# Optimization experiments

Measured on AMD Instinct MI355X. Metric: run time of the kernel, lower is better.

Reference implementation:

```python
import jax, jax.numpy as jnp
import numpy as np

N_NODES = 100000
N_EDGES = 1600000
HEADS = 4
HID = 64
IN_CH = 3
N_GRAPHS = 64
NEG_SLOPE = 0.2  # PyG GATConv default


def _gat_layer(x, src, dst, W, a_src, a_dst, b):
    """PyG GATConv with concat=False (head-mean), eval mode (no dropout)."""
    N = x.shape[0]
    xl = (x @ W).reshape(N, HEADS, HID)            # [N,H,C]
    es = (xl * a_src).sum(-1)                       # [N,H] alpha_src
    ed = (xl * a_dst).sum(-1)                       # [N,H] alpha_dst
    e = jax.nn.leaky_relu(es[src] + ed[dst], NEG_SLOPE)  # [E,H]
    # segment softmax over incoming edges of each dst node
    m = jax.ops.segment_max(e, dst, num_segments=N)      # [N,H]
    ex = jnp.exp(e - m[dst])
    s = jax.ops.segment_sum(ex, dst, num_segments=N)     # [N,H]
    alpha = ex / s[dst]                                   # [E,H]
    msg = xl[src] * alpha[:, :, None]                     # [E,H,C]
    out = jax.ops.segment_sum(msg, dst, num_segments=N)   # [N,H,C]
    return out.mean(axis=1) + b                            # head mean + bias


def setup_inputs() -> dict:
    key = jax.random.key(0)
    ks = jax.random.split(key, 12)
    x = jax.random.normal(ks[0], (N_NODES, IN_CH), dtype=jnp.float32)
    edge_index = jax.random.randint(ks[1], (2, N_EDGES), 0, N_NODES, dtype=jnp.int64)
    batch_ids = jnp.sort(jax.random.randint(ks[2], (N_NODES,), 0, N_GRAPHS, dtype=jnp.int64))
    def glorot(k, shape, fan_in):
        return jax.random.normal(k, shape, dtype=jnp.float32) / np.sqrt(fan_in)
    W1 = glorot(ks[3], (IN_CH, HEADS * HID), IN_CH)
    a_src1 = glorot(ks[4], (HEADS, HID), HID)
    a_dst1 = glorot(ks[5], (HEADS, HID), HID)
    b1 = jnp.zeros((HID,), dtype=jnp.float32)
    W2 = glorot(ks[6], (HID, HEADS * HID), HID)
    a_src2 = glorot(ks[7], (HEADS, HID), HID)
    a_dst2 = glorot(ks[8], (HEADS, HID), HID)
    b2 = jnp.zeros((HID,), dtype=jnp.float32)
    return {"x": x, "edge_index": edge_index, "batch_ids": batch_ids,
            "W1": W1, "a_src1": a_src1, "a_dst1": a_dst1, "b1": b1,
            "W2": W2, "a_src2": a_src2, "a_dst2": a_dst2, "b2": b2}


def reference(x, edge_index, batch_ids, W1, a_src1, a_dst1, b1, W2, a_src2, a_dst2, b2):
    src, dst = edge_index[0], edge_index[1]
    h = jax.nn.relu(_gat_layer(x, src, dst, W1, a_src1, a_dst1, b1))
    h = jax.nn.relu(_gat_layer(h, src, dst, W2, a_src2, a_dst2, b2))
    # global_add_pool
    g = jax.ops.segment_sum(h, batch_ids, num_segments=N_GRAPHS)  # [G, HID]
    return g
```

## Files before the change

kernel.cpp:

```cpp
#include <hip/hip_runtime.h>
#include <math.h>

#define HEADS 4
#define HID 64
#define BSHIFT 7
#define BWIDTH 128
#define CCAP 4096
#define DCHUNK 8192

typedef __attribute__((ext_vector_type(8))) short short8;
typedef __attribute__((ext_vector_type(4))) float f32x4;
typedef __attribute__((ext_vector_type(2))) float f32x2;

__device__ __forceinline__ float lrelu(float x) { return x > 0.f ? x : 0.2f * x; }

__device__ __forceinline__ unsigned short bf16r(float f) {
    unsigned u = __float_as_uint(f);
    unsigned r = (u + 0x7FFFu + ((u >> 16) & 1u)) >> 16;
    return (unsigned short)r;
}
__device__ __forceinline__ f32x2 unpk(unsigned u) {
    f32x2 r;
    r.x = __uint_as_float(u << 16);
    r.y = __uint_as_float(u & 0xffff0000u);
    return r;
}

__device__ __forceinline__ float wred_sum(float v) {
#pragma unroll
    for (int o = 32; o > 0; o >>= 1) v += __shfl_xor(v, o);
    return v;
}
__device__ __forceinline__ float red16_sum(float v) {
#pragma unroll
    for (int o = 8; o > 0; o >>= 1) v += __shfl_xor(v, o);
    return v;
}

__global__ void k_bhist(const int* __restrict__ dstI, int* __restrict__ bcnt,
                        int E, int NBUCK) {
    __shared__ int h[1024];
    for (int i = threadIdx.x; i < NBUCK; i += 256) h[i] = 0;
    __syncthreads();
    int stride = gridDim.x * 256;
    for (int e = blockIdx.x * 256 + threadIdx.x; e < E; e += stride)
        atomicAdd(&h[dstI[e] >> BSHIFT], 1);
    __syncthreads();
    for (int i = threadIdx.x; i < NBUCK; i += 256)
        if (h[i]) atomicAdd(&bcnt[i], h[i]);
}

__global__ void k_bscan(const int* __restrict__ bcnt, int* __restrict__ bbase,
                        int* __restrict__ gcur, int* __restrict__ off,
                        int NBUCK, int N, int E) {
    __shared__ int lds[1024];
    int t = threadIdx.x;
    int v = (t < NBUCK) ? bcnt[t] : 0;
    lds[t] = v;
    __syncthreads();
    for (int s = 1; s < 1024; s <<= 1) {
        int u = (t >= s) ? lds[t - s] : 0;
        __syncthreads();
        lds[t] += u;
        __syncthreads();
    }
    if (t < NBUCK) {
        int b = lds[t] - v;
        bbase[t] = b;
        gcur[t] = b;
    }
    if (t == 0) { bbase[NBUCK] = E; off[N] = E; }
}

__global__ void k_bdist(const int* __restrict__ srcI, const int* __restrict__ dstI,
                        int* __restrict__ gcur, unsigned* __restrict__ pairs,
                        int E, int NBUCK) {
    __shared__ int h[1024];
    __shared__ int cur[1024];
    for (int i = threadIdx.x; i < NBUCK; i += 1024) h[i] = 0;
    __syncthreads();
    int base = blockIdx.x * DCHUNK;
    int sr[8], dr[8];
#pragma unroll
    for (int k = 0; k < 8; k++) {
        int e = base + threadIdx.x + k * 1024;
        if (e < E) {
            sr[k] = srcI[e];
            dr[k] = dstI[e];
            atomicAdd(&h[dr[k] >> BSHIFT], 1);
        } else dr[k] = -1;
    }
    __syncthreads();
    for (int i = threadIdx.x; i < NBUCK; i += 1024)
        cur[i] = h[i] ? atomicAdd(&gcur[i], h[i]) : 0;
    __syncthreads();
#pragma unroll
    for (int k = 0; k < 8; k++) {
        if (dr[k] >= 0) {
            int b = dr[k] >> BSHIFT;
            int p = atomicAdd(&cur[b], 1);
            pairs[p] = ((unsigned)sr[k] << BSHIFT) | ((unsigned)dr[k] & (BWIDTH - 1));
        }
    }
}

__global__ void k_bcsr(const unsigned* __restrict__ pairs, const int* __restrict__ bbase,
                       int* __restrict__ off, int* __restrict__ csr, int N) {
    __shared__ int cnt[BWIDTH];
    __shared__ int scan[BWIDTH];
    __shared__ int cur[BWIDTH];
    __shared__ int stage[CCAP];
    int b = blockIdx.x;
    int nodeBase = b << BSHIFT;
    int nNodes = N - nodeBase;
    if (nNodes > BWIDTH) nNodes = BWIDTH;
    int e0 = bbase[b], e1 = bbase[b + 1];
    int ecnt = e1 - e0;
    if (threadIdx.x < BWIDTH) cnt[threadIdx.x] = 0;
    __syncthreads();
    for (int i = threadIdx.x; i < ecnt; i += 256)
        atomicAdd(&cnt[pairs[e0 + i] & (BWIDTH - 1)], 1);
    __syncthreads();
    if (threadIdx.x < BWIDTH)
        scan[threadIdx.x] = (threadIdx.x < nNodes) ? cnt[threadIdx.x] : 0;
    __syncthreads();
    for (int s = 1; s < BWIDTH; s <<= 1) {
        int u = 0;
        if (threadIdx.x < BWIDTH && threadIdx.x >= s) u = scan[threadIdx.x - s];
        __syncthreads();
        if (threadIdx.x < BWIDTH) scan[threadIdx.x] += u;
        __syncthreads();
    }
    if (threadIdx.x < nNodes) {
        int ex = scan[threadIdx.x] - cnt[threadIdx.x];
        off[nodeBase + threadIdx.x] = e0 + ex;
        cur[threadIdx.x] = ex;
    }
    __syncthreads();
    for (int i = threadIdx.x; i < ecnt; i += 256) {
        unsigned pr = pairs[e0 + i];
        int l = atomicAdd(&cur[pr & (BWIDTH - 1)], 1);
        int src = (int)(pr >> BSHIFT);
        if (l < CCAP) stage[l] = src;
        else csr[e0 + l] = src;
    }
    __syncthreads();
    int lim = ecnt < CCAP ? ecnt : CCAP;
    for (int i = threadIdx.x; i < lim; i += 256) csr[e0 + i] = stage[i];
}

__device__ __forceinline__ void prep_body(const float* __restrict__ W,
                                          const float* __restrict__ asrc,
                                          const float* __restrict__ adst,
                                          float* __restrict__ p_src,
                                          float* __restrict__ p_dst, int K, int blk) {
    int wid = blk * 4 + (threadIdx.x >> 6);
    int lane = threadIdx.x & 63;
    int total = K * 4 * 2;
    if (wid >= total) return;
    int which = wid / (K * 4);
    int hk = wid % (K * 4);
    int h = hk / K, k = hk % K;
    const float* a = which ? adst : asrc;
    float v = W[(size_t)k * 256 + h * 64 + lane] * a[h * 64 + lane];
    v = wred_sum(v);
    if (lane == 0) (which ? p_dst : p_src)[h * K + k] = v;
}

__global__ void k_prep_all(const float* __restrict__ W1, const float* __restrict__ as1,
                           const float* __restrict__ ad1, const float* __restrict__ W2,
                           const float* __restrict__ as2, const float* __restrict__ ad2,
                           float* __restrict__ p1s, float* __restrict__ p1d,
                           float* __restrict__ qs, float* __restrict__ qd,
                           unsigned short* __restrict__ W2bt, float* __restrict__ out,
                           int outTotal) {
    int b = blockIdx.x;
    if (b < 6) {
        prep_body(W1, as1, ad1, p1s, p1d, 3, b);
    } else if (b < 134) {
        prep_body(W2, as2, ad2, qs, qd, 64, b - 6);
    } else {
        int i = (b - 134) * 256 + threadIdx.x;
        int c = i >> 8, kh = i & 255;
        int h = kh >> 6, kf = kh & 63;
        W2bt[i] = bf16r(W2[kf * 256 + h * 64 + c]);
        if (i < outTotal) out[i] = 0.f;
    }
}

__global__ void k_agg1(const int* __restrict__ off, const int* __restrict__ csr,
                       const float* __restrict__ x, const float* __restrict__ ps,
                       const float* __restrict__ pd, const float* __restrict__ W1,
                       const float* __restrict__ b1, const float* __restrict__ qs,
                       const float* __restrict__ qd, unsigned short* __restrict__ houtb,
                       float* __restrict__ es2, float* __restrict__ ed2, int N) {
    int grp = (blockIdx.x * blockDim.x + threadIdx.x) >> 4;
    int l = threadIdx.x & 15;
    int wid = grp;
    bool active = wid < N;
    int o0 = 0, deg = 0;
    float ed0 = 0.f, ed1 = 0.f, ed2v = 0.f, ed3 = 0.f;
    if (active) {
        o0 = off[wid];
        deg = off[wid + 1] - o0;
        float y0 = x[wid * 3], y1 = x[wid * 3 + 1], y2 = x[wid * 3 + 2];
        ed0 = y0 * pd[0] + y1 * pd[1] + y2 * pd[2];
        ed1 = y0 * pd[3] + y1 * pd[4] + y2 * pd[5];
        ed2v = y0 * pd[6] + y1 * pd[7] + y2 * pd[8];
        ed3 = y0 * pd[9] + y1 * pd[10] + y2 * pd[11];
    }

    float t0 = 0.f, t1 = 0.f, t2 = 0.f, t3 = 0.f;
    float a00 = 0, a01 = 0, a02 = 0, a10 = 0, a11 = 0, a12 = 0;
    float a20 = 0, a21 = 0, a22 = 0, a30 = 0, a31 = 0, a32 = 0;
    for (int j = l; j < deg; j += 16) {
        int s = csr[o0 + j];
        float xv0 = x[s * 3], xv1 = x[s * 3 + 1], xv2 = x[s * 3 + 2];
        float e0 = __expf(lrelu(xv0 * ps[0] + xv1 * ps[1] + xv2 * ps[2] + ed0));
        float e1 = __expf(lrelu(xv0 * ps[3] + xv1 * ps[4] + xv2 * ps[5] + ed1));
        float e2 = __expf(lrelu(xv0 * ps[6] + xv1 * ps[7] + xv2 * ps[8] + ed2v));
        float e3 = __expf(lrelu(xv0 * ps[9] + xv1 * ps[10] + xv2 * ps[11] + ed3));
        t0 += e0; t1 += e1; t2 += e2; t3 += e3;
        a00 += e0 * xv0; a01 += e0 * xv1; a02 += e0 * xv2;
        a10 += e1 * xv0; a11 += e1 * xv1; a12 += e1 * xv2;
        a20 += e2 * xv0; a21 += e2 * xv1; a22 += e2 * xv2;
        a30 += e3 * xv0; a31 += e3 * xv1; a32 += e3 * xv2;
    }
    t0 = red16_sum(t0); t1 = red16_sum(t1); t2 = red16_sum(t2); t3 = red16_sum(t3);
    float i0 = t0 > 0.f ? 1.f / t0 : 0.f;
    float i1 = t1 > 0.f ? 1.f / t1 : 0.f;
    float i2 = t2 > 0.f ? 1.f / t2 : 0.f;
    float i3 = t3 > 0.f ? 1.f / t3 : 0.f;
    a00 = red16_sum(a00) * i0; a01 = red16_sum(a01) * i0; a02 = red16_sum(a02) * i0;
    a10 = red16_sum(a10) * i1; a11 = red16_sum(a11) * i1; a12 = red16_sum(a12) * i1;
    a20 = red16_sum(a20) * i2; a21 = red16_sum(a21) * i2; a22 = red16_sum(a22) * i2;
    a30 = red16_sum(a30) * i3; a31 = red16_sum(a31) * i3; a32 = red16_sum(a32) * i3;

    if (!active) return;

    const float4* W1f = (const float4*)W1;
    float4 r = make_float4(0.f, 0.f, 0.f, 0.f);
    float ah[4][3] = {{a00, a01, a02}, {a10, a11, a12}, {a20, a21, a22}, {a30, a31, a32}};
#pragma unroll
    for (int k = 0; k < 3; k++) {
#pragma unroll
        for (int h = 0; h < 4; h++) {
            float4 wv = W1f[k * 64 + h * 16 + l];
            float a = ah[h][k];
            r.x += a * wv.x; r.y += a * wv.y; r.z += a * wv.z; r.w += a * wv.w;
        }
    }
    float4 bv = ((const float4*)b1)[l];
    float4 hv;
    hv.x = fmaxf(0.25f * r.x + bv.x, 0.f);
    hv.y = fmaxf(0.25f * r.y + bv.y, 0.f);
    hv.z = fmaxf(0.25f * r.z + bv.z, 0.f);
    hv.w = fmaxf(0.25f * r.w + bv.w, 0.f);
    ((ushort4*)houtb)[(size_t)wid * 16 + l] =
        make_ushort4(bf16r(hv.x), bf16r(hv.y), bf16r(hv.z), bf16r(hv.w));

    const float4* qsf = (const float4*)qs;
    const float4* qdf = (const float4*)qd;
    float psv[4], pdv[4];
#pragma unroll
    for (int h = 0; h < 4; h++) {
        float4 q = qsf[h * 16 + l];
        psv[h] = red16_sum(hv.x * q.x + hv.y * q.y + hv.z * q.z + hv.w * q.w);
        float4 p = qdf[h * 16 + l];
        pdv[h] = red16_sum(hv.x * p.x + hv.y * p.y + hv.z * p.z + hv.w * p.w);
    }
    if (l == 0) {
        ((float4*)es2)[wid] = make_float4(psv[0], psv[1], psv[2], psv[3]);
        ((float4*)ed2)[wid] = make_float4(pdv[0], pdv[1], pdv[2], pdv[3]);
    }
}

#define NS 16
__global__ void k_agg2(const int* __restrict__ off, const int* __restrict__ csr,
                       const float* __restrict__ es, const float* __restrict__ ed,
                       const unsigned short* __restrict__ houtb,
                       unsigned short* __restrict__ aggb, int N) {
    __shared__ float exl[NS * 64 * 4];
    __shared__ int   sl[NS * 64];
    __shared__ float minv[NS * 4];
    __shared__ int   meta[NS * 2];

    int l = threadIdx.x & 15;
    int slot = threadIdx.x >> 4;
    int wid = blockIdx.x * NS + slot;
    bool active = wid < N;
    int o0 = 0, deg = 0;
    float4 edv = make_float4(0.f, 0.f, 0.f, 0.f);
    if (active) {
        o0 = off[wid];
        deg = off[wid + 1] - o0;
        edv = ((const float4*)ed)[wid];
    }

    float t0 = 0.f, t1 = 0.f, t2 = 0.f, t3 = 0.f;
    for (int j = l; j < deg; j += 16) {
        int s = csr[o0 + j];
        float4 ev = ((const float4*)es)[s];
        float e0 = __expf(lrelu(ev.x + edv.x));
        float e1 = __expf(lrelu(ev.y + edv.y));
        float e2 = __expf(lrelu(ev.z + edv.z));
        float e3 = __expf(lrelu(ev.w + edv.w));
        if (j < 64) {
            ((float4*)exl)[slot * 64 + j] = make_float4(e0, e1, e2, e3);
            sl[slot * 64 + j] = s;
        }
        t0 += e0; t1 += e1; t2 += e2; t3 += e3;
    }
    {
        int dmain = deg < 64 ? deg : 64;
        int d8 = (dmain + 7) & ~7;
        if (dmain + l < d8) {
            ((float4*)exl)[slot * 64 + dmain + l] = make_float4(0.f, 0.f, 0.f, 0.f);
            sl[slot * 64 + dmain + l] = 0;
        }
    }
    t0 = red16_sum(t0); t1 = red16_sum(t1); t2 = red16_sum(t2); t3 = red16_sum(t3);
    if (l == 0) {
        minv[slot * 4 + 0] = t0 > 0.f ? 1.f / t0 : 0.f;
        minv[slot * 4 + 1] = t1 > 0.f ? 1.f / t1 : 0.f;
        minv[slot * 4 + 2] = t2 > 0.f ? 1.f / t2 : 0.f;
        minv[slot * 4 + 3] = t3 > 0.f ? 1.f / t3 : 0.f;
        meta[slot * 2 + 0] = o0;
        meta[slot * 2 + 1] = deg;
    }
    __syncthreads();

    int lane = threadIdx.x & 63;
    int w = threadIdx.x >> 6;
    int half = lane >> 5;
    int c2 = lane & 31;
    for (int sidx = 0; sidx < 4; sidx++) {
        int slot2 = w * 4 + sidx;
        int nd = blockIdx.x * NS + slot2;
        if (nd >= N) continue;
        int o0b = meta[slot2 * 2 + 0], degb = meta[slot2 * 2 + 1];
        float iv0 = minv[slot2 * 4 + 0], iv1 = minv[slot2 * 4 + 1];
        float iv2 = minv[slot2 * 4 + 2], iv3 = minv[slot2 * 4 + 3];

        f32x2 q0 = {0.f, 0.f}, q1 = {0.f, 0.f}, q2 = {0.f, 0.f}, q3 = {0.f, 0.f};
        const float4* EX = ((const float4*)exl) + slot2 * 64;
        const int* S = sl + slot2 * 64;
        int dmain = degb < 64 ? degb : 64;
        int d8 = (dmain + 7) & ~7;
        for (int j = 0; j < d8; j += 8) {
            float4 a0 = EX[j + half];
            float4 a1 = EX[j + 2 + half];
            float4 a2 = EX[j + 4 + half];
            float4 a3 = EX[j + 6 + half];
            int s0 = S[j + half], s1 = S[j + 2 + half];
            int s2 = S[j + 4 + half], s3 = S[j + 6 + half];
            unsigned u0 = *(const unsigned*)(houtb + (size_t)s0 * 64 + 2 * c2);
            unsigned u1 = *(const unsigned*)(houtb + (size_t)s1 * 64 + 2 * c2);
            unsigned u2 = *(const unsigned*)(houtb + (size_t)s2 * 64 + 2 * c2);
            unsigned u3 = *(const unsigned*)(houtb + (size_t)s3 * 64 + 2 * c2);
            f32x2 v0 = unpk(u0), v1 = unpk(u1), v2 = unpk(u2), v3 = unpk(u3);
            q0 += a0.x * v0; q0 += a1.x * v1; q0 += a2.x * v2; q0 += a3.x * v3;
            q1 += a0.y * v0; q1 += a1.y * v1; q1 += a2.y * v2; q1 += a3.y * v3;
            q2 += a0.z * v0; q2 += a1.z * v1; q2 += a2.z * v2; q2 += a3.z * v3;
            q3 += a0.w * v0; q3 += a1.w * v1; q3 += a2.w * v2; q3 += a3.w * v3;
        }
        if (degb > 64) {
            float4 edv2 = ((const float4*)ed)[nd];
            for (int j = 64 + half; j < degb; j += 2) {
                int s = csr[o0b + j];
                float4 ev = ((const float4*)es)[s];
                float e0 = __expf(lrelu(ev.x + edv2.x));
                float e1 = __expf(lrelu(ev.y + edv2.y));
                float e2 = __expf(lrelu(ev.z + edv2.z));
                float e3 = __expf(lrelu(ev.w + edv2.w));
                unsigned u = *(const unsigned*)(houtb + (size_t)s * 64 + 2 * c2);
                f32x2 v = unpk(u);
                q0 += e0 * v; q1 += e1 * v; q2 += e2 * v; q3 += e3 * v;
            }
        }
        q0.x += __shfl_xor(q0.x, 32); q0.y += __shfl_xor(q0.y, 32);
        q1.x += __shfl_xor(q1.x, 32); q1.y += __shfl_xor(q1.y, 32);
        q2.x += __shfl_xor(q2.x, 32); q2.y += __shfl_xor(q2.y, 32);
        q3.x += __shfl_xor(q3.x, 32); q3.y += __shfl_xor(q3.y, 32);

        if (half == 0) {
            size_t b = (size_t)nd * 256;
            unsigned w0 = (unsigned)bf16r(q0.x * iv0) | ((unsigned)bf16r(q0.y * iv0) << 16);
            unsigned w1 = (unsigned)bf16r(q1.x * iv1) | ((unsigned)bf16r(q1.y * iv1) << 16);
            unsigned w2 = (unsigned)bf16r(q2.x * iv2) | ((unsigned)bf16r(q2.y * iv2) << 16);
            unsigned w3 = (unsigned)bf16r(q3.x * iv3) | ((unsigned)bf16r(q3.y * iv3) << 16);
            *(unsigned*)(aggb + b + 2 * c2)        = w0;
            *(unsigned*)(aggb + b + 64 + 2 * c2)   = w1;
            *(unsigned*)(aggb + b + 128 + 2 * c2)  = w2;
            *(unsigned*)(aggb + b + 192 + 2 * c2)  = w3;
        }
    }
}

__global__ void k_out2(const unsigned short* __restrict__ aggb,
                       const unsigned short* __restrict__ W2bt,
                       const float* __restrict__ b2, const int* __restrict__ batch,
                       float* __restrict__ out, int N) {
    int w = threadIdx.x >> 6, lane = threadIdx.x & 63;
    int nodeBase = blockIdx.x * 64 + w * 16;
    int m = lane & 15;
    int quad = lane >> 4;
    const short* A = (const short*)aggb + (size_t)(nodeBase + m) * 256 + quad * 8;
    const short* B = (const short*)W2bt;

    f32x4 acc0 = {0.f, 0.f, 0.f, 0.f}, acc1 = {0.f, 0.f, 0.f, 0.f};
    f32x4 acc2 = {0.f, 0.f, 0.f, 0.f}, acc3 = {0.f, 0.f, 0.f, 0.f};
#pragma unroll
    for (int kk = 0; kk < 8; kk++) {
        short8 af = *(const short8*)(A + kk * 32);
        short8 b0 = *(const short8*)(B + (size_t)(0 * 16 + m) * 256 + kk * 32 + quad * 8);
        short8 b1v = *(const short8*)(B + (size_t)(1 * 16 + m) * 256 + kk * 32 + quad * 8);
        short8 b2v = *(const short8*)(B + (size_t)(2 * 16 + m) * 256 + kk * 32 + quad * 8);
        short8 b3v = *(const short8*)(B + (size_t)(3 * 16 + m) * 256 + kk * 32 + quad * 8);
        acc0 = __builtin_amdgcn_mfma_f32_16x16x32_bf16(af, b0, acc0, 0, 0, 0);
        acc1 = __builtin_amdgcn_mfma_f32_16x16x32_bf16(af, b1v, acc1, 0, 0, 0);
        acc2 = __builtin_amdgcn_mfma_f32_16x16x32_bf16(af, b2v, acc2, 0, 0, 0);
        acc3 = __builtin_amdgcn_mfma_f32_16x16x32_bf16(af, b3v, acc3, 0, 0, 0);
    }
    f32x4 accs[4] = {acc0, acc1, acc2, acc3};

    float vals[4][4];
#pragma unroll
    for (int cb = 0; cb < 4; cb++) {
        float bv = b2[cb * 16 + m];
#pragma unroll
        for (int r = 0; r < 4; r++)
            vals[cb][r] = fmaxf(0.25f * accs[cb][r] + bv, 0.f);
    }

    bool fast = (nodeBase + 15 < N);
    int g0 = 0;
    if (fast) {
        g0 = batch[nodeBase];
        int g1 = batch[nodeBase + 15];
        fast = (g0 == g1);
    }
    if (fast) {
#pragma unroll
        for (int cb = 0; cb < 4; cb++) {
            float s = vals[cb][0] + vals[cb][1] + vals[cb][2] + vals[cb][3];
            s += __shfl_xor(s, 16);
            s += __shfl_xor(s, 32);
            if (quad == 0) atomicAdd(&out[g0 * 64 + cb * 16 + m], s);
        }
    } else {
#pragma unroll
        for (int r = 0; r < 4; r++) {
            int node = nodeBase + quad * 4 + r;
            if (node < N) {
                int g = batch[node];
#pragma unroll
                for (int cb = 0; cb < 4; cb++)
                    atomicAdd(&out[g * 64 + cb * 16 + m], vals[cb][r]);
            }
        }
    }
}

extern "C" void kernel_launch(void* const* d_in, const int* in_sizes, int n_in,
                              void* d_out, int out_size, void* d_ws, size_t ws_size,
                              hipStream_t stream) {
    const float* x   = (const float*)d_in[0];
    const int*   ei  = (const int*)d_in[1];
    const int*   bat = (const int*)d_in[2];
    const float* W1  = (const float*)d_in[3];
    const float* as1 = (const float*)d_in[4];
    const float* ad1 = (const float*)d_in[5];
    const float* b1  = (const float*)d_in[6];
    const float* W2  = (const float*)d_in[7];
    const float* as2 = (const float*)d_in[8];
    const float* ad2 = (const float*)d_in[9];
    const float* b2  = (const float*)d_in[10];
    float* out = (float*)d_out;

    int N = in_sizes[0] / 3;
    int E = in_sizes[1] / 2;
    int G = out_size / 64;
    const int* srcI = ei;
    const int* dstI = ei + E;
    int NBUCK = (N + BWIDTH - 1) >> BSHIFT;

    float* fw = (float*)d_ws;
    size_t fo = 0;
    unsigned short* aggb = (unsigned short*)fw; fo += (size_t)N * 128;
    unsigned short* houtb = (unsigned short*)(fw + fo); fo += (size_t)N * 32;
    float* esB   = fw + fo; fo += (size_t)N * 4;
    float* edB   = fw + fo; fo += (size_t)N * 4;
    float* p1s   = fw + fo; fo += 64;
    float* p1d   = fw + fo; fo += 64;
    float* qs    = fw + fo; fo += 256;
    float* qd    = fw + fo; fo += 256;
    unsigned short* W2bt = (unsigned short*)(fw + fo); fo += 64 * 256 / 2;
    int* iw = (int*)(fw + fo);
    size_t io = 0;
    unsigned* pairs = (unsigned*)iw; io += E;
    int* csr    = iw + io; io += E;
    int* off    = iw + io; io += N + 1;
    int* bbase  = iw + io; io += 1025;
    int* gcur   = iw + io; io += 1024;
    int* bcnt   = iw + io; io += 1024;

    int nGrpBlk = (N + 15) / 16;

    hipMemsetAsync(bcnt, 0, 1024 * sizeof(int), stream);
    k_bhist<<<256, 256, 0, stream>>>(dstI, bcnt, E, NBUCK);
    k_bscan<<<1, 1024, 0, stream>>>(bcnt, bbase, gcur, off, NBUCK, N, E);
    k_bdist<<<(E + DCHUNK - 1) / DCHUNK, 1024, 0, stream>>>(srcI, dstI, gcur, pairs, E, NBUCK);
    k_bcsr<<<NBUCK, 256, 0, stream>>>(pairs, bbase, off, csr, N);

    k_prep_all<<<198, 256, 0, stream>>>(W1, as1, ad1, W2, as2, ad2,
                                        p1s, p1d, qs, qd, W2bt, out, G * 64);

    k_agg1<<<nGrpBlk, 256, 0, stream>>>(off, csr, x, p1s, p1d, W1, b1, qs, qd,
                                        houtb, esB, edB, N);

    k_agg2<<<nGrpBlk, 256, 0, stream>>>(off, csr, esB, edB, houtb, aggb, N);
    k_out2<<<(N + 63) / 64, 256, 0, stream>>>(aggb, W2bt, b2, bat, out, N);
}
```

Baseline: 247.8 us.

## Fuse layer-2 aggregation with output MFMA projection via shared memory

Merges k_out2 into k_agg2. Each block's 16 aggregated node rows now stay in padded shared memory instead of being written to a global bf16 buffer and read back. After a block barrier, one wavefront runs the MFMA projection, bias, relu and pooling for those 16 nodes. This removes the global round trip of the aggregate (about 51 MB) and one kernel launch. In exchange, three of the four waves sit idle during the projection phase, and shared-memory use per block grows.

```diff
diff --git a/kernel.cpp b/kernel.cpp
--- a/kernel.cpp
+++ b/kernel.cpp
@@ -7,6 +7,7 @@
 #define BWIDTH 128
 #define CCAP 4096
 #define DCHUNK 8192
+#define APAD 264
 
 typedef __attribute__((ext_vector_type(8))) short short8;
 typedef __attribute__((ext_vector_type(4))) float f32x4;
@@ -279,11 +280,14 @@
 __global__ void k_agg2(const int* __restrict__ off, const int* __restrict__ csr,
                        const float* __restrict__ es, const float* __restrict__ ed,
                        const unsigned short* __restrict__ houtb,
-                       unsigned short* __restrict__ aggb, int N) {
+                       const unsigned short* __restrict__ W2bt,
+                       const float* __restrict__ b2, const int* __restrict__ batch,
+                       float* __restrict__ out, int N) {
     __shared__ float exl[NS * 64 * 4];
     __shared__ int   sl[NS * 64];
     __shared__ float minv[NS * 4];
     __shared__ int   meta[NS * 2];
+    __shared__ unsigned short aggl[NS * APAD];
 
     int l = threadIdx.x & 15;
     int slot = threadIdx.x >> 4;
@@ -318,6 +322,10 @@
             ((float4*)exl)[slot * 64 + dmain + l] = make_float4(0.f, 0.f, 0.f, 0.f);
             sl[slot * 64 + dmain + l] = 0;
         }
+    }
+    if (!active) {
+        for (int i = l; i < 128; i += 16)
+            ((unsigned*)(aggl + slot * APAD))[i] = 0u;
     }
     t0 = red16_sum(t0); t1 = red16_sum(t1); t2 = red16_sum(t2); t3 = red16_sum(t3);
     if (l == 0) {
@@ -384,28 +392,24 @@
         q3.x += __shfl_xor(q3.x, 32); q3.y += __shfl_xor(q3.y, 32);
 
         if (half == 0) {
-            size_t b = (size_t)nd * 256;
+            unsigned short* arow = aggl + slot2 * APAD;
             unsigned w0 = (unsigned)bf16r(q0.x * iv0) | ((unsigned)bf16r(q0.y * iv0) << 16);
             unsigned w1 = (unsigned)bf16r(q1.x * iv1) | ((unsigned)bf16r(q1.y * iv1) << 16);
             unsigned w2 = (unsigned)bf16r(q2.x * iv2) | ((unsigned)bf16r(q2.y * iv2) << 16);
             unsigned w3 = (unsigned)bf16r(q3.x * iv3) | ((unsigned)bf16r(q3.y * iv3) << 16);
-            *(unsigned*)(aggb + b + 2 * c2)        = w0;
-            *(unsigned*)(aggb + b + 64 + 2 * c2)   = w1;
-            *(unsigned*)(aggb + b + 128 + 2 * c2)  = w2;
-            *(unsigned*)(aggb + b + 192 + 2 * c2)  = w3;
-        }
-    }
-}
-
-__global__ void k_out2(const unsigned short* __restrict__ aggb,
-                       const unsigned short* __restrict__ W2bt,
-                       const float* __restrict__ b2, const int* __restrict__ batch,
-                       float* __restrict__ out, int N) {
-    int w = threadIdx.x >> 6, lane = threadIdx.x & 63;
-    int nodeBase = blockIdx.x * 64 + w * 16;
+            *(unsigned*)(arow + 2 * c2)        = w0;
+            *(unsigned*)(arow + 64 + 2 * c2)   = w1;
+            *(unsigned*)(arow + 128 + 2 * c2)  = w2;
+            *(unsigned*)(arow + 192 + 2 * c2)  = w3;
+        }
+    }
+    __syncthreads();
+
+    if (w != 0) return;
+    int nodeBase = blockIdx.x * NS;
     int m = lane & 15;
     int quad = lane >> 4;
-    const short* A = (const short*)aggb + (size_t)(nodeBase + m) * 256 + quad * 8;
+    const short* A = (const short*)aggl + m * APAD + quad * 8;
     const short* B = (const short*)W2bt;
 
     f32x4 acc0 = {0.f, 0.f, 0.f, 0.f}, acc1 = {0.f, 0.f, 0.f, 0.f};
@@ -487,8 +491,7 @@
 
     float* fw = (float*)d_ws;
     size_t fo = 0;
-    unsigned short* aggb = (unsigned short*)fw; fo += (size_t)N * 128;
-    unsigned short* houtb = (unsigned short*)(fw + fo); fo += (size_t)N * 32;
+    unsigned short* houtb = (unsigned short*)fw; fo += (size_t)N * 32;
     float* esB   = fw + fo; fo += (size_t)N * 4;
     float* edB   = fw + fo; fo += (size_t)N * 4;
     float* p1s   = fw + fo; fo += 64;
@@ -519,6 +522,5 @@
     k_agg1<<<nGrpBlk, 256, 0, stream>>>(off, csr, x, p1s, p1d, W1, b1, qs, qd,
                                         houtb, esB, edB, N);
 
-    k_agg2<<<nGrpBlk, 256, 0, stream>>>(off, csr, esB, edB, houtb, aggb, N);
-    k_out2<<<(N + 63) / 64, 256, 0, stream>>>(aggb, W2bt, b2, bat, out, N);
-}
+    k_agg2<<<nGrpBlk, 256, 0, stream>>>(off, csr, esB, edB, houtb, W2bt, b2, bat, out, N);
+}
```

Measured after the change: 238.7 us. -3.7%, faster.
